# Kernel tuning notes

Hardware: AMD Instinct MI355X
Metric: run time of the kernel (lower is better)

Reference implementation:

```python
import jax, jax.numpy as jnp
import numpy as np

N = 512          # number of spins
BATCH = 1024     # number of spin configurations
NUM_PAIRS = N * (N - 1) // 2  # C(N,2) = 130816


def _make_pairs(n):
    # itertools.combinations(range(n), 2) in lexicographic order == upper-tri indices
    i, j = np.triu_indices(n, k=1)
    return jnp.asarray(np.stack([i, j], axis=1), dtype=jnp.int32)  # [C, 2]


def setup_inputs() -> dict:
    key = jax.random.key(0)
    kx, k1, k2 = jax.random.split(key, 3)
    # spin configurations: +/-1 (Ising spins), float32
    x = jnp.where(jax.random.bernoulli(kx, 0.5, (BATCH, N)), 1.0, -1.0).astype(jnp.float32)
    # couplings initialized like the flax module: 0.0001 * normal
    J1 = 1e-4 * jax.random.normal(k1, (N,), dtype=jnp.float32)
    J2 = 1e-4 * jax.random.normal(k2, (NUM_PAIRS,), dtype=jnp.float32)
    pairs = _make_pairs(N)  # [C, 2] int32, constant combinatorial structure
    return {"x": x, "J1": J1, "J2": J2, "pairs": pairs}


def reference(x, J1, J2, pairs):
    # energy = x @ J1 + sum_c J2[c] * x[:, c0] * x[:, c1]
    # Fused gather + elementwise product replaces the unrolled per-combination loop.
    energy = x @ J1                                   # [B]
    z = x[:, pairs[:, 0]] * x[:, pairs[:, 1]]         # [B, C]
    energy = energy + z @ J2                          # [B]
    return energy
```

## Files before the change

### kernel.cpp

```cpp
#include <hip/hip_runtime.h>

#define NSP   512
#define BATCH 1024

typedef __attribute__((ext_vector_type(8))) short bf16x8;
typedef __attribute__((ext_vector_type(4))) float f32x4;

__device__ __forceinline__ unsigned short f2bf(float f) {
    union { float f; unsigned int u; } c; c.f = f;
    unsigned int u = c.u + (0x7FFFu + ((c.u >> 16) & 1u));
    return (unsigned short)(u >> 16);
}

__global__ __launch_bounds__(256) void prep(const float* __restrict__ x,
                                            const float* __restrict__ J2,
                                            unsigned short* __restrict__ Mt,
                                            unsigned short* __restrict__ xb,
                                            float* __restrict__ energy) {
    int idx = blockIdx.x * 256 + threadIdx.x;
    int j = idx >> 9;
    int i = idx & (NSP - 1);
    float v = 0.0f;
    if (i < j) v = J2[i * (NSP - 1) - (i * (i - 1)) / 2 + (j - i - 1)];
    Mt[idx] = f2bf(v);
    if (idx < (BATCH * NSP) / 4) {
        float4 xv = reinterpret_cast<const float4*>(x)[idx];
        ushort4 o;
        o.x = f2bf(xv.x); o.y = f2bf(xv.y); o.z = f2bf(xv.z); o.w = f2bf(xv.w);
        reinterpret_cast<ushort4*>(xb)[idx] = o;
    }
    if (idx < BATCH) energy[idx] = 0.0f;
}

__global__ __launch_bounds__(256) void ising_mfma(const float* __restrict__ x,
                                                  const float* __restrict__ J1,
                                                  const unsigned short* __restrict__ Mt,
                                                  const unsigned short* __restrict__ xb,
                                                  float* __restrict__ energy) {
    const int tid  = threadIdx.x;
    const int w    = tid >> 6;
    const int lane = tid & 63;
    const int bt   = blockIdx.x;
    const int jt   = blockIdx.y * 4 + w;
    const int b0   = bt * 16;
    const int j0   = jt * 16;
    const int r16  = lane & 15;
    const int kg   = lane >> 4;

    const int nch = (16 * jt + 46) >> 5;

    const unsigned short* Ap = xb + (size_t)(b0 + r16) * NSP + kg * 8;
    const unsigned short* Bp = Mt + (size_t)(j0 + r16) * NSP + kg * 8;

    f32x4 acc = {0.0f, 0.0f, 0.0f, 0.0f};
    #pragma unroll 4
    for (int ch = 0; ch < nch; ++ch) {
        bf16x8 a = *reinterpret_cast<const bf16x8*>(Ap + ch * 32);
        bf16x8 b = *reinterpret_cast<const bf16x8*>(Bp + ch * 32);
        acc = __builtin_amdgcn_mfma_f32_16x16x32_bf16(a, b, acc, 0, 0, 0);
    }

    const int jcol = j0 + r16;
    const float j1 = J1[jcol];
    float part[4];
    #pragma unroll
    for (int r = 0; r < 4; ++r) {
        int row = kg * 4 + r;
        float xw = x[(size_t)(b0 + row) * NSP + jcol];
        part[r] = xw * (acc[r] + j1);
    }
    #pragma unroll
    for (int off = 8; off >= 1; off >>= 1)
        #pragma unroll
        for (int r = 0; r < 4; ++r)
            part[r] += __shfl_xor(part[r], off, 64);

    if (r16 == 0) {
        #pragma unroll
        for (int r = 0; r < 4; ++r)
            atomicAdd(&energy[b0 + kg * 4 + r], part[r]);
    }
}

extern "C" void kernel_launch(void* const* d_in, const int* in_sizes, int n_in,
                              void* d_out, int out_size, void* d_ws, size_t ws_size,
                              hipStream_t stream) {
    const float* x  = (const float*)d_in[0];
    const float* J1 = (const float*)d_in[1];
    const float* J2 = (const float*)d_in[2];
    unsigned short* Mt = (unsigned short*)d_ws;
    unsigned short* xb = (unsigned short*)((char*)d_ws + 524288);
    float* energy = (float*)d_out;

    prep<<<dim3((NSP * NSP) / 256), 256, 0, stream>>>(x, J2, Mt, xb, energy);
    ising_mfma<<<dim3(BATCH / 16, 8), 256, 0, stream>>>(x, J1, Mt, xb, energy);
}
```

Measured before the change: 67.95 us.

## Tile prep transpose through shared memory and reduce atomics per block

The prep kernel now builds the transposed bf16 coupling matrix in 64x64 tiles staged in shared memory. J2 is read row-contiguously and Mt is written with 16-byte vector stores, replacing the old strided gather. Tiles below the diagonal are skipped, and the x-to-bf16 conversion is spread over fewer, larger blocks. The MFMA kernel combines the four waves' partial energies in shared memory before issuing one atomic per row, cutting atomic traffic. The risks are that 64 prep blocks leave much of the GPU idle, and that the skipped lower tiles of Mt are never written.

```diff
diff --git a/kernel.cpp b/kernel.cpp
--- a/kernel.cpp
+++ b/kernel.cpp
@@ -5,6 +5,7 @@
 
 typedef __attribute__((ext_vector_type(8))) short bf16x8;
 typedef __attribute__((ext_vector_type(4))) float f32x4;
+typedef __attribute__((ext_vector_type(8))) unsigned short u16x8;
 
 __device__ __forceinline__ unsigned short f2bf(float f) {
     union { float f; unsigned int u; } c; c.f = f;
@@ -17,19 +18,48 @@
                                             unsigned short* __restrict__ Mt,
                                             unsigned short* __restrict__ xb,
                                             float* __restrict__ energy) {
-    int idx = blockIdx.x * 256 + threadIdx.x;
-    int j = idx >> 9;
-    int i = idx & (NSP - 1);
-    float v = 0.0f;
-    if (i < j) v = J2[i * (NSP - 1) - (i * (i - 1)) / 2 + (j - i - 1)];
-    Mt[idx] = f2bf(v);
-    if (idx < (BATCH * NSP) / 4) {
-        float4 xv = reinterpret_cast<const float4*>(x)[idx];
-        ushort4 o;
-        o.x = f2bf(xv.x); o.y = f2bf(xv.y); o.z = f2bf(xv.z); o.w = f2bf(xv.w);
-        reinterpret_cast<ushort4*>(xb)[idx] = o;
+    __shared__ float tile[64][65];
+    const int t  = threadIdx.x;
+    const int ti = blockIdx.x >> 3;
+    const int tj = blockIdx.x & 7;
+
+    {
+        const float4* x4 = reinterpret_cast<const float4*>(x);
+        int base = blockIdx.x * 256 + t;
+        #pragma unroll
+        for (int e = 0; e < 8; ++e) {
+            float4 v = x4[base + 16384 * e];
+            ushort4 o; o.x = f2bf(v.x); o.y = f2bf(v.y); o.z = f2bf(v.z); o.w = f2bf(v.w);
+            reinterpret_cast<ushort4*>(xb)[base + 16384 * e] = o;
+        }
     }
-    if (idx < BATCH) energy[idx] = 0.0f;
+    if (blockIdx.x == 8) {
+        float4 z = {0.0f, 0.0f, 0.0f, 0.0f};
+        reinterpret_cast<float4*>(energy)[t] = z;
+    }
+    if (ti > tj) return;
+
+    const int i0 = ti * 64, j0 = tj * 64;
+    #pragma unroll
+    for (int e = 0; e < 16; ++e) {
+        int n = t + 256 * e;
+        int r = n >> 6, cc = n & 63;
+        int i = i0 + r, j = j0 + cc;
+        float v = 0.0f;
+        if (i < j) v = J2[i * (NSP - 1) - (i * (i - 1)) / 2 + (j - i - 1)];
+        tile[r][cc] = v;
+    }
+    __syncthreads();
+    {
+        int jr = t >> 2;
+        int s  = (t & 3) * 16;
+        unsigned short o[16];
+        #pragma unroll
+        for (int e = 0; e < 16; ++e) o[e] = f2bf(tile[s + e][jr]);
+        u16x8* dst = reinterpret_cast<u16x8*>(Mt + (size_t)(j0 + jr) * NSP + i0 + s);
+        dst[0] = *reinterpret_cast<u16x8*>(o);
+        dst[1] = *reinterpret_cast<u16x8*>(o + 8);
+    }
 }
 
 __global__ __launch_bounds__(256) void ising_mfma(const float* __restrict__ x,
@@ -37,6 +67,7 @@
                                                   const unsigned short* __restrict__ Mt,
                                                   const unsigned short* __restrict__ xb,
                                                   float* __restrict__ energy) {
+    __shared__ float red[4][16];
     const int tid  = threadIdx.x;
     const int w    = tid >> 6;
     const int lane = tid & 63;
@@ -65,8 +96,7 @@
     float part[4];
     #pragma unroll
     for (int r = 0; r < 4; ++r) {
-        int row = kg * 4 + r;
-        float xw = x[(size_t)(b0 + row) * NSP + jcol];
+        float xw = x[(size_t)(b0 + kg * 4 + r) * NSP + jcol];
         part[r] = xw * (acc[r] + j1);
     }
     #pragma unroll
@@ -77,8 +107,12 @@
 
     if (r16 == 0) {
         #pragma unroll
-        for (int r = 0; r < 4; ++r)
-            atomicAdd(&energy[b0 + kg * 4 + r], part[r]);
+        for (int r = 0; r < 4; ++r) red[w][kg * 4 + r] = part[r];
+    }
+    __syncthreads();
+    if (tid < 16) {
+        float s = red[0][tid] + red[1][tid] + red[2][tid] + red[3][tid];
+        atomicAdd(&energy[b0 + tid], s);
     }
 }
 
@@ -92,6 +126,6 @@
     unsigned short* xb = (unsigned short*)((char*)d_ws + 524288);
     float* energy = (float*)d_out;
 
-    prep<<<dim3((NSP * NSP) / 256), 256, 0, stream>>>(x, J2, Mt, xb, energy);
+    prep<<<dim3(64), 256, 0, stream>>>(x, J2, Mt, xb, energy);
     ising_mfma<<<dim3(BATCH / 16, 8), 256, 0, stream>>>(x, J1, Mt, xb, energy);
 }
```

After: 73.14 us. 1.08x slower.
